# Kernel optimization log

Hardware: AMD Instinct MI355X
Metric: run time of the kernel (lower is better)

## Reference

```python
import jax, jax.numpy as jnp
import numpy as np

BATCH = 16
N_ROIS = 1000
NUM_CLASSES = 81
DET_MAX = 100
MIN_CONF = 0.7
NMS_THRESH = 0.3
BBOX_STD = jnp.array([0.1, 0.1, 0.2, 0.2], jnp.float32)


def setup_inputs() -> dict:
    key = jax.random.key(0)
    k1, k2, k3, k4, k5 = jax.random.split(key, 5)
    # valid normalized boxes (y1,x1,y2,x2) with y2>y1, x2>x1
    y1 = jax.random.uniform(k1, (BATCH, N_ROIS, 1)) * 0.7
    x1 = jax.random.uniform(k2, (BATCH, N_ROIS, 1)) * 0.7
    hw = jax.random.uniform(k3, (BATCH, N_ROIS, 2)) * 0.28 + 0.02
    rois = jnp.concatenate([y1, x1, y1 + hw[..., :1], x1 + hw[..., 1:]], axis=-1)
    fpn_class = jax.nn.softmax(jax.random.normal(k4, (BATCH, N_ROIS, NUM_CLASSES)) * 2.0, axis=-1)
    fpn_bbox = jax.random.normal(k5, (BATCH, N_ROIS, NUM_CLASSES, 4)) * 0.1
    window = jnp.tile(jnp.array([[0.0, 0.0, 1.0, 1.0]], jnp.float32), (BATCH, 1))
    return {"rois": rois, "fpn_class": fpn_class, "fpn_bbox": fpn_bbox, "window": window}


def apply_box_deltas(boxes, deltas):
    # boxes [N,4] (y1,x1,y2,x2), deltas [N,4] (dy,dx,log dh,log dw)
    h = boxes[:, 2] - boxes[:, 0]
    w = boxes[:, 3] - boxes[:, 1]
    cy = boxes[:, 0] + 0.5 * h
    cx = boxes[:, 1] + 0.5 * w
    cy = cy + deltas[:, 0] * h
    cx = cx + deltas[:, 1] * w
    h = h * jnp.exp(deltas[:, 2])
    w = w * jnp.exp(deltas[:, 3])
    y1 = cy - 0.5 * h
    x1 = cx - 0.5 * w
    return jnp.stack([y1, x1, y1 + h, x1 + w], axis=1)


def clip_boxes(boxes, window):
    wy1, wx1, wy2, wx2 = window[0], window[1], window[2], window[3]
    y1 = jnp.clip(boxes[:, 0], wy1, wy2)
    x1 = jnp.clip(boxes[:, 1], wx1, wx2)
    y2 = jnp.clip(boxes[:, 2], wy1, wy2)
    x2 = jnp.clip(boxes[:, 3], wx1, wx2)
    return jnp.stack([y1, x1, y2, x2], axis=1)


def box_iou(a, b):
    # a [N,4], b [M,4] -> [N,M]
    y1 = jnp.maximum(a[:, None, 0], b[None, :, 0])
    x1 = jnp.maximum(a[:, None, 1], b[None, :, 1])
    y2 = jnp.minimum(a[:, None, 2], b[None, :, 2])
    x2 = jnp.minimum(a[:, None, 3], b[None, :, 3])
    inter = jnp.maximum(y2 - y1, 0.0) * jnp.maximum(x2 - x1, 0.0)
    area_a = (a[:, 2] - a[:, 0]) * (a[:, 3] - a[:, 1])
    area_b = (b[:, 2] - b[:, 0]) * (b[:, 3] - b[:, 1])
    union = area_a[:, None] + area_b[None, :] - inter
    return inter / jnp.maximum(union, 1e-10)


def per_class_nms_mask(boxes, class_ids, scores):
    """boxes [N,4], class_ids [N] int, scores [N] (already -1 where pre-filtered).
    Returns bool [N]: survives greedy per-class NMS (max DET_MAX kept per class)."""
    fg = jnp.arange(1, NUM_CLASSES)                       # [C-1] skip background
    sc = jnp.where(class_ids[None, :] == fg[:, None], scores[None, :], -1.0)  # [C-1,N]
    order = jnp.argsort(-sc, axis=1)                      # [C-1,N] score-desc per class
    iou = box_iou(boxes, boxes)                           # [N,N]
    col = jnp.arange(N_ROIS)
    active0 = sc >= 0.0
    kept0 = jnp.zeros_like(active0)
    cnt0 = jnp.zeros((NUM_CLASSES - 1,), jnp.int32)

    def body(i, carry):
        active, kept, cnt = carry
        cur = order[:, i]                                  # [C-1] current box idx per class
        is_act = jnp.take_along_axis(active, cur[:, None], axis=1)[:, 0]
        is_kept = is_act & (cnt < DET_MAX)
        cnt = cnt + is_kept.astype(jnp.int32)
        kept = kept | ((col[None, :] == cur[:, None]) & is_kept[:, None])
        suppress = is_kept[:, None] & (iou[cur] > NMS_THRESH)  # [C-1,N]
        active = active & ~suppress
        return (active, kept, cnt)

    _, kept, _ = jax.lax.fori_loop(0, N_ROIS, body, (active0, kept0, cnt0))
    return kept.any(axis=0)


def _refine_one(rois, probs, deltas, window):
    n = jnp.arange(N_ROIS)
    class_ids = jnp.argmax(probs, axis=1)                 # [N]
    class_scores = probs[n, class_ids]                    # [N]
    d = deltas[n, class_ids] * BBOX_STD                   # [N,4]
    refined = clip_boxes(apply_box_deltas(rois, d), window)
    keep = (class_ids > 0) & (class_scores >= MIN_CONF)
    sg = jax.lax.stop_gradient
    nms_keep = per_class_nms_mask(
        sg(refined), class_ids, jnp.where(keep, sg(class_scores), -1.0))
    keep = keep & nms_keep
    sf = jnp.where(keep, class_scores, -1.0)
    top_s, top_i = jax.lax.top_k(sf, DET_MAX)             # keep top DET_MAX overall
    valid = top_s >= 0.0
    det = jnp.concatenate(
        [refined[top_i],
         class_ids[top_i][:, None].astype(jnp.float32),
         class_scores[top_i][:, None]], axis=1)           # [DET_MAX,6]
    return jnp.where(valid[:, None], det, 0.0)            # zero-pad invalid rows


def reference(rois, fpn_class, fpn_bbox, window):
    # [B, DET_MAX, 6] = (y1,x1,y2,x2,class_id,score), normalized coords
    return jax.vmap(_refine_one)(rois, fpn_class, fpn_bbox, window)
```

## Files before the change

### kernel.cpp

```cpp
#include <hip/hip_runtime.h>
#include <math.h>

#define BATCH 16
#define N_ROIS 1000
#define NUM_CLASSES 81
#define DET_MAX 100
#define MIN_CONF 0.7f
#define NMS_THRESH 0.3f

#define ROI_TILE 128
#define CMAX N_ROIS

__global__ __launch_bounds__(256) void refine_v2(
    const float* __restrict__ rois, const float* __restrict__ probs,
    const float* __restrict__ deltas, const float* __restrict__ window,
    float* __restrict__ ws_box, float* __restrict__ ws_score, int* __restrict__ ws_cls)
{
    __shared__ float s_probs[ROI_TILE * NUM_CLASSES];

    const int tile = blockIdx.x;
    const int base_roi = tile * ROI_TILE;

    const float4* src = (const float4*)(probs + (size_t)base_roi * NUM_CLASSES);
    float4* dst = (float4*)s_probs;
    for (int i = threadIdx.x; i < ROI_TILE * NUM_CLASSES / 4; i += 256)
        dst[i] = src[i];
    __syncthreads();

    if (threadIdx.x < ROI_TILE) {
        const int idx = base_roi + threadIdx.x;
        const int b = idx / N_ROIS;

        const float* p = s_probs + threadIdx.x * NUM_CLASSES;
        int best = 0;
        float bs = p[0];
        for (int c = 1; c < NUM_CLASSES; ++c) {
            float v = p[c];
            if (v > bs) { bs = v; best = c; }
        }

        const float4 dd = ((const float4*)deltas)[(size_t)idx * NUM_CLASSES + best];
        float dy = dd.x * 0.1f, dx = dd.y * 0.1f, dh = dd.z * 0.2f, dw = dd.w * 0.2f;

        const float4 rr = ((const float4*)rois)[idx];
        float y1 = rr.x, x1 = rr.y, y2 = rr.z, x2 = rr.w;
        float h = y2 - y1, w = x2 - x1;
        float cy = y1 + 0.5f * h, cx = x1 + 0.5f * w;
        cy += dy * h;
        cx += dx * w;
        h *= expf(dh);
        w *= expf(dw);
        float ny1 = cy - 0.5f * h;
        float nx1 = cx - 0.5f * w;
        float ny2 = ny1 + h;
        float nx2 = nx1 + w;

        const float* win = window + b * 4;
        float wy1 = win[0], wx1 = win[1], wy2 = win[2], wx2 = win[3];
        ny1 = fminf(fmaxf(ny1, wy1), wy2);
        nx1 = fminf(fmaxf(nx1, wx1), wx2);
        ny2 = fminf(fmaxf(ny2, wy1), wy2);
        nx2 = fminf(fmaxf(nx2, wx1), wx2);

        bool keep = (best > 0) && (bs >= MIN_CONF);

        float4* wbx = (float4*)ws_box;
        wbx[idx] = make_float4(ny1, nx1, ny2, nx2);
        ws_score[idx] = keep ? bs : -1.0f;
        ws_cls[idx] = best;
    }
}

__global__ __launch_bounds__(256) void nms_topk_v2(
    const float* __restrict__ ws_box, const float* __restrict__ ws_score,
    const int* __restrict__ ws_cls, float* __restrict__ out)
{
    const int b = blockIdx.x;
    const int tid = threadIdx.x;

    __shared__ float s_cbox[CMAX][4];
    __shared__ float s_csc[CMAX];
    __shared__ short s_cidx[CMAX];
    __shared__ unsigned char s_ccls[CMAX];
    __shared__ float s_sbox[CMAX][4];
    __shared__ float s_ssc[CMAX];
    __shared__ unsigned char s_scls[CMAX];
    __shared__ unsigned char s_supp[CMAX];
    __shared__ unsigned char s_kept[CMAX];
    __shared__ short s_slot[CMAX];
    __shared__ int s_cnt[NUM_CLASSES];
    __shared__ int s_C;

    if (tid == 0) s_C = 0;
    if (tid < NUM_CLASSES) s_cnt[tid] = 0;

    for (int i = tid; i < DET_MAX * 6; i += 256)
        out[(size_t)b * DET_MAX * 6 + i] = 0.0f;
    __syncthreads();

    for (int i = tid; i < N_ROIS; i += 256) {
        float sc = ws_score[b * N_ROIS + i];
        if (sc >= 0.0f) {
            int k = atomicAdd(&s_C, 1);
            s_csc[k] = sc;
            s_cidx[k] = (short)i;
            s_ccls[k] = (unsigned char)ws_cls[b * N_ROIS + i];
            float4 bb = ((const float4*)ws_box)[b * N_ROIS + i];
            s_cbox[k][0] = bb.x; s_cbox[k][1] = bb.y;
            s_cbox[k][2] = bb.z; s_cbox[k][3] = bb.w;
        }
    }
    __syncthreads();
    const int C = s_C;

    for (int k = tid; k < C; k += 256) {
        float sk = s_csc[k];
        int ik = s_cidx[k];
        int rank = 0;
        for (int j = 0; j < C; ++j) {
            float sj = s_csc[j];
            rank += (sj > sk) | ((sj == sk) & (s_cidx[j] < ik));
        }
        s_ssc[rank] = sk;
        s_scls[rank] = s_ccls[k];
        s_sbox[rank][0] = s_cbox[k][0];
        s_sbox[rank][1] = s_cbox[k][1];
        s_sbox[rank][2] = s_cbox[k][2];
        s_sbox[rank][3] = s_cbox[k][3];
        s_supp[rank] = 0;
        s_kept[rank] = 0;
        s_slot[rank] = 0;
    }
    __syncthreads();

    if (tid < 64) {
        int total = 0;
        for (int i = 0; i < C; ++i) {
            if (s_supp[i]) continue;
            int c = s_scls[i];
            int cn = s_cnt[c];
            if (cn >= DET_MAX) continue;
            s_cnt[c] = cn + 1;
            if (tid == 0) { s_kept[i] = 1; s_slot[i] = (short)total; }
            ++total;
            float a0 = s_sbox[i][0], a1 = s_sbox[i][1];
            float a2 = s_sbox[i][2], a3 = s_sbox[i][3];
            float area_a = (a2 - a0) * (a3 - a1);
            for (int j = i + 1 + tid; j < C; j += 64) {
                if (s_supp[j] || s_scls[j] != c) continue;
                float b0 = s_sbox[j][0], b1 = s_sbox[j][1];
                float b2 = s_sbox[j][2], b3 = s_sbox[j][3];
                float yy1 = fmaxf(a0, b0);
                float xx1 = fmaxf(a1, b1);
                float yy2 = fminf(a2, b2);
                float xx2 = fminf(a3, b3);
                float inter = fmaxf(yy2 - yy1, 0.0f) * fmaxf(xx2 - xx1, 0.0f);
                float area_b = (b2 - b0) * (b3 - b1);
                float uni = area_a + area_b - inter;
                float iou = inter / fmaxf(uni, 1e-10f);
                if (iou > NMS_THRESH) s_supp[j] = 1;
            }
            if (total == DET_MAX) break;
        }
    }
    __syncthreads();

    for (int i = tid; i < C; i += 256) {
        if (s_kept[i]) {
            int slot = s_slot[i];
            float* o = out + (size_t)b * DET_MAX * 6 + slot * 6;
            o[0] = s_sbox[i][0];
            o[1] = s_sbox[i][1];
            o[2] = s_sbox[i][2];
            o[3] = s_sbox[i][3];
            o[4] = (float)s_scls[i];
            o[5] = s_ssc[i];
        }
    }
}

extern "C" void kernel_launch(void* const* d_in, const int* in_sizes, int n_in,
                              void* d_out, int out_size, void* d_ws, size_t ws_size,
                              hipStream_t stream) {
    const float* rois      = (const float*)d_in[0];
    const float* fpn_class = (const float*)d_in[1];
    const float* fpn_bbox  = (const float*)d_in[2];
    const float* window    = (const float*)d_in[3];
    float* out = (float*)d_out;

    float* ws_box   = (float*)d_ws;
    float* ws_score = ws_box + (size_t)BATCH * N_ROIS * 4;
    int*   ws_cls   = (int*)(ws_score + (size_t)BATCH * N_ROIS);

    refine_v2<<<BATCH * N_ROIS / ROI_TILE, 256, 0, stream>>>(
        rois, fpn_class, fpn_bbox, window, ws_box, ws_score, ws_cls);
    nms_topk_v2<<<BATCH, 256, 0, stream>>>(ws_box, ws_score, ws_cls, out);
}
```

Baseline: 94.99 us.

## Fuse refine and NMS into one per-batch kernel with tiled probs staging

Merges the per-roi refinement kernel into the NMS kernel so each batch item is processed by one 1024-thread block that streams class probabilities through shared memory in tiles. Box refinement and delta loads are skipped for rois that fail the confidence filter, and the global workspace round trip and second launch are removed. The cost is much less parallelism for the bandwidth-heavy argmax stage, since only 16 blocks read all probabilities with per-tile barriers.

```diff
diff --git a/kernel.cpp b/kernel.cpp
--- a/kernel.cpp
+++ b/kernel.cpp
@@ -8,112 +8,97 @@
 #define MIN_CONF 0.7f
 #define NMS_THRESH 0.3f
 
-#define ROI_TILE 128
-#define CMAX N_ROIS
+#define TILE_ROIS 200
+#define N_TILES (N_ROIS / TILE_ROIS)
+#define TILE_F4 (TILE_ROIS * NUM_CLASSES / 4)
+#define BLOCK 1024
 
-__global__ __launch_bounds__(256) void refine_v2(
+__global__ __launch_bounds__(BLOCK) void detection_fused(
     const float* __restrict__ rois, const float* __restrict__ probs,
     const float* __restrict__ deltas, const float* __restrict__ window,
-    float* __restrict__ ws_box, float* __restrict__ ws_score, int* __restrict__ ws_cls)
-{
-    __shared__ float s_probs[ROI_TILE * NUM_CLASSES];
-
-    const int tile = blockIdx.x;
-    const int base_roi = tile * ROI_TILE;
-
-    const float4* src = (const float4*)(probs + (size_t)base_roi * NUM_CLASSES);
-    float4* dst = (float4*)s_probs;
-    for (int i = threadIdx.x; i < ROI_TILE * NUM_CLASSES / 4; i += 256)
-        dst[i] = src[i];
-    __syncthreads();
-
-    if (threadIdx.x < ROI_TILE) {
-        const int idx = base_roi + threadIdx.x;
-        const int b = idx / N_ROIS;
-
-        const float* p = s_probs + threadIdx.x * NUM_CLASSES;
-        int best = 0;
-        float bs = p[0];
-        for (int c = 1; c < NUM_CLASSES; ++c) {
-            float v = p[c];
-            if (v > bs) { bs = v; best = c; }
-        }
-
-        const float4 dd = ((const float4*)deltas)[(size_t)idx * NUM_CLASSES + best];
-        float dy = dd.x * 0.1f, dx = dd.y * 0.1f, dh = dd.z * 0.2f, dw = dd.w * 0.2f;
-
-        const float4 rr = ((const float4*)rois)[idx];
-        float y1 = rr.x, x1 = rr.y, y2 = rr.z, x2 = rr.w;
-        float h = y2 - y1, w = x2 - x1;
-        float cy = y1 + 0.5f * h, cx = x1 + 0.5f * w;
-        cy += dy * h;
-        cx += dx * w;
-        h *= expf(dh);
-        w *= expf(dw);
-        float ny1 = cy - 0.5f * h;
-        float nx1 = cx - 0.5f * w;
-        float ny2 = ny1 + h;
-        float nx2 = nx1 + w;
-
-        const float* win = window + b * 4;
-        float wy1 = win[0], wx1 = win[1], wy2 = win[2], wx2 = win[3];
-        ny1 = fminf(fmaxf(ny1, wy1), wy2);
-        nx1 = fminf(fmaxf(nx1, wx1), wx2);
-        ny2 = fminf(fmaxf(ny2, wy1), wy2);
-        nx2 = fminf(fmaxf(nx2, wx1), wx2);
-
-        bool keep = (best > 0) && (bs >= MIN_CONF);
-
-        float4* wbx = (float4*)ws_box;
-        wbx[idx] = make_float4(ny1, nx1, ny2, nx2);
-        ws_score[idx] = keep ? bs : -1.0f;
-        ws_cls[idx] = best;
-    }
-}
-
-__global__ __launch_bounds__(256) void nms_topk_v2(
-    const float* __restrict__ ws_box, const float* __restrict__ ws_score,
-    const int* __restrict__ ws_cls, float* __restrict__ out)
+    float* __restrict__ out)
 {
     const int b = blockIdx.x;
     const int tid = threadIdx.x;
 
-    __shared__ float s_cbox[CMAX][4];
-    __shared__ float s_csc[CMAX];
-    __shared__ short s_cidx[CMAX];
-    __shared__ unsigned char s_ccls[CMAX];
-    __shared__ float s_sbox[CMAX][4];
-    __shared__ float s_ssc[CMAX];
-    __shared__ unsigned char s_scls[CMAX];
-    __shared__ unsigned char s_supp[CMAX];
-    __shared__ unsigned char s_kept[CMAX];
-    __shared__ short s_slot[CMAX];
+    __shared__ float s_tile[TILE_ROIS * NUM_CLASSES];
+    __shared__ float s_cbox[N_ROIS][4];
+    __shared__ float s_csc[N_ROIS];
+    __shared__ short s_cidx[N_ROIS];
+    __shared__ unsigned char s_ccls[N_ROIS];
+    __shared__ float s_sbox[N_ROIS][4];
+    __shared__ float s_ssc[N_ROIS];
+    __shared__ unsigned char s_scls[N_ROIS];
+    __shared__ unsigned char s_supp[N_ROIS];
+    __shared__ unsigned char s_kept[N_ROIS];
+    __shared__ short s_slot[N_ROIS];
     __shared__ int s_cnt[NUM_CLASSES];
     __shared__ int s_C;
 
     if (tid == 0) s_C = 0;
     if (tid < NUM_CLASSES) s_cnt[tid] = 0;
 
-    for (int i = tid; i < DET_MAX * 6; i += 256)
+    for (int i = tid; i < DET_MAX * 6; i += BLOCK)
         out[(size_t)b * DET_MAX * 6 + i] = 0.0f;
-    __syncthreads();
 
-    for (int i = tid; i < N_ROIS; i += 256) {
-        float sc = ws_score[b * N_ROIS + i];
-        if (sc >= 0.0f) {
-            int k = atomicAdd(&s_C, 1);
-            s_csc[k] = sc;
-            s_cidx[k] = (short)i;
-            s_ccls[k] = (unsigned char)ws_cls[b * N_ROIS + i];
-            float4 bb = ((const float4*)ws_box)[b * N_ROIS + i];
-            s_cbox[k][0] = bb.x; s_cbox[k][1] = bb.y;
-            s_cbox[k][2] = bb.z; s_cbox[k][3] = bb.w;
+    const float* win = window + b * 4;
+    const float wy1 = win[0], wx1 = win[1], wy2 = win[2], wx2 = win[3];
+
+    const float4* pbase = (const float4*)(probs + (size_t)b * N_ROIS * NUM_CLASSES);
+
+    for (int t = 0; t < N_TILES; ++t) {
+        const float4* src = pbase + (size_t)t * TILE_F4;
+        float4* dst = (float4*)s_tile;
+        for (int i = tid; i < TILE_F4; i += BLOCK)
+            dst[i] = src[i];
+        __syncthreads();
+
+        if (tid < TILE_ROIS) {
+            const int r = t * TILE_ROIS + tid;
+            const float* p = s_tile + tid * NUM_CLASSES;
+            int best = 0;
+            float bs = p[0];
+            for (int c = 1; c < NUM_CLASSES; ++c) {
+                float v = p[c];
+                if (v > bs) { bs = v; best = c; }
+            }
+
+            if (best > 0 && bs >= MIN_CONF) {
+                const int gidx = b * N_ROIS + r;
+                const float4 dd = ((const float4*)deltas)[(size_t)gidx * NUM_CLASSES + best];
+                float dy = dd.x * 0.1f, dx = dd.y * 0.1f, dh = dd.z * 0.2f, dw = dd.w * 0.2f;
+
+                const float4 rr = ((const float4*)rois)[gidx];
+                float y1 = rr.x, x1 = rr.y, y2 = rr.z, x2 = rr.w;
+                float h = y2 - y1, w = x2 - x1;
+                float cy = y1 + 0.5f * h, cx = x1 + 0.5f * w;
+                cy += dy * h;
+                cx += dx * w;
+                h *= expf(dh);
+                w *= expf(dw);
+                float ny1 = cy - 0.5f * h;
+                float nx1 = cx - 0.5f * w;
+                float ny2 = ny1 + h;
+                float nx2 = nx1 + w;
+
+                ny1 = fminf(fmaxf(ny1, wy1), wy2);
+                nx1 = fminf(fmaxf(nx1, wx1), wx2);
+                ny2 = fminf(fmaxf(ny2, wy1), wy2);
+                nx2 = fminf(fmaxf(nx2, wx1), wx2);
+
+                int k = atomicAdd(&s_C, 1);
+                s_cbox[k][0] = ny1; s_cbox[k][1] = nx1;
+                s_cbox[k][2] = ny2; s_cbox[k][3] = nx2;
+                s_csc[k] = bs;
+                s_cidx[k] = (short)r;
+                s_ccls[k] = (unsigned char)best;
+            }
         }
+        __syncthreads();
     }
-    __syncthreads();
     const int C = s_C;
 
-    for (int k = tid; k < C; k += 256) {
+    for (int k = tid; k < C; k += BLOCK) {
         float sk = s_csc[k];
         int ik = s_cidx[k];
         int rank = 0;
@@ -157,18 +142,16 @@
                 float inter = fmaxf(yy2 - yy1, 0.0f) * fmaxf(xx2 - xx1, 0.0f);
                 float area_b = (b2 - b0) * (b3 - b1);
                 float uni = area_a + area_b - inter;
-                float iou = inter / fmaxf(uni, 1e-10f);
-                if (iou > NMS_THRESH) s_supp[j] = 1;
+                if (inter / fmaxf(uni, 1e-10f) > NMS_THRESH) s_supp[j] = 1;
             }
             if (total == DET_MAX) break;
         }
     }
     __syncthreads();
 
-    for (int i = tid; i < C; i += 256) {
+    for (int i = tid; i < C; i += BLOCK) {
         if (s_kept[i]) {
-            int slot = s_slot[i];
-            float* o = out + (size_t)b * DET_MAX * 6 + slot * 6;
+            float* o = out + (size_t)b * DET_MAX * 6 + s_slot[i] * 6;
             o[0] = s_sbox[i][0];
             o[1] = s_sbox[i][1];
             o[2] = s_sbox[i][2];
@@ -188,11 +171,6 @@
     const float* window    = (const float*)d_in[3];
     float* out = (float*)d_out;
 
-    float* ws_box   = (float*)d_ws;
-    float* ws_score = ws_box + (size_t)BATCH * N_ROIS * 4;
-    int*   ws_cls   = (int*)(ws_score + (size_t)BATCH * N_ROIS);
-
-    refine_v2<<<BATCH * N_ROIS / ROI_TILE, 256, 0, stream>>>(
-        rois, fpn_class, fpn_bbox, window, ws_box, ws_score, ws_cls);
-    nms_topk_v2<<<BATCH, 256, 0, stream>>>(ws_box, ws_score, ws_cls, out);
+    detection_fused<<<BATCH, BLOCK, 0, stream>>>(
+        rois, fpn_class, fpn_bbox, window, out);
 }
```

After: 102.6 us. 1.08x slower.

## Parallelize NMS across classes with per-class buckets and skip refine for dropped ROIs

Applied to the files above, without the earlier changes.

The serial greedy NMS loop, run by one wavefront over all candidates, is replaced by per-class buckets: a prefix sum gives class offsets, and each class runs its own NMS on one thread against earlier kept boxes in the same class. Output slots come from counting kept entries before each index. The refine kernel now computes and stores boxes and class only for ROIs that pass the confidence filter, which avoids the gather from the deltas tensor for dropped ROIs. Within a class the work is serial per thread and the bucket fill scans all candidates, so load imbalance between classes is possible.

```diff
diff --git a/kernel.cpp b/kernel.cpp
--- a/kernel.cpp
+++ b/kernel.cpp
@@ -9,17 +9,15 @@
 #define NMS_THRESH 0.3f
 
 #define ROI_TILE 128
-#define CMAX N_ROIS
-
-__global__ __launch_bounds__(256) void refine_v2(
+
+__global__ __launch_bounds__(256) void refine_v3(
     const float* __restrict__ rois, const float* __restrict__ probs,
     const float* __restrict__ deltas, const float* __restrict__ window,
     float* __restrict__ ws_box, float* __restrict__ ws_score, int* __restrict__ ws_cls)
 {
     __shared__ float s_probs[ROI_TILE * NUM_CLASSES];
 
-    const int tile = blockIdx.x;
-    const int base_roi = tile * ROI_TILE;
+    const int base_roi = blockIdx.x * ROI_TILE;
 
     const float4* src = (const float4*)(probs + (size_t)base_roi * NUM_CLASSES);
     float4* dst = (float4*)s_probs;
@@ -39,56 +37,57 @@
             if (v > bs) { bs = v; best = c; }
         }
 
-        const float4 dd = ((const float4*)deltas)[(size_t)idx * NUM_CLASSES + best];
-        float dy = dd.x * 0.1f, dx = dd.y * 0.1f, dh = dd.z * 0.2f, dw = dd.w * 0.2f;
-
-        const float4 rr = ((const float4*)rois)[idx];
-        float y1 = rr.x, x1 = rr.y, y2 = rr.z, x2 = rr.w;
-        float h = y2 - y1, w = x2 - x1;
-        float cy = y1 + 0.5f * h, cx = x1 + 0.5f * w;
-        cy += dy * h;
-        cx += dx * w;
-        h *= expf(dh);
-        w *= expf(dw);
-        float ny1 = cy - 0.5f * h;
-        float nx1 = cx - 0.5f * w;
-        float ny2 = ny1 + h;
-        float nx2 = nx1 + w;
-
-        const float* win = window + b * 4;
-        float wy1 = win[0], wx1 = win[1], wy2 = win[2], wx2 = win[3];
-        ny1 = fminf(fmaxf(ny1, wy1), wy2);
-        nx1 = fminf(fmaxf(nx1, wx1), wx2);
-        ny2 = fminf(fmaxf(ny2, wy1), wy2);
-        nx2 = fminf(fmaxf(nx2, wx1), wx2);
-
-        bool keep = (best > 0) && (bs >= MIN_CONF);
-
-        float4* wbx = (float4*)ws_box;
-        wbx[idx] = make_float4(ny1, nx1, ny2, nx2);
+        const bool keep = (best > 0) && (bs >= MIN_CONF);
         ws_score[idx] = keep ? bs : -1.0f;
-        ws_cls[idx] = best;
+
+        if (keep) {
+            const float4 dd = ((const float4*)deltas)[(size_t)idx * NUM_CLASSES + best];
+            float dy = dd.x * 0.1f, dx = dd.y * 0.1f, dh = dd.z * 0.2f, dw = dd.w * 0.2f;
+
+            const float4 rr = ((const float4*)rois)[idx];
+            float y1 = rr.x, x1 = rr.y, y2 = rr.z, x2 = rr.w;
+            float h = y2 - y1, w = x2 - x1;
+            float cy = y1 + 0.5f * h, cx = x1 + 0.5f * w;
+            cy += dy * h;
+            cx += dx * w;
+            h *= expf(dh);
+            w *= expf(dw);
+            float ny1 = cy - 0.5f * h;
+            float nx1 = cx - 0.5f * w;
+            float ny2 = ny1 + h;
+            float nx2 = nx1 + w;
+
+            const float* win = window + b * 4;
+            float wy1 = win[0], wx1 = win[1], wy2 = win[2], wx2 = win[3];
+            ny1 = fminf(fmaxf(ny1, wy1), wy2);
+            nx1 = fminf(fmaxf(nx1, wx1), wx2);
+            ny2 = fminf(fmaxf(ny2, wy1), wy2);
+            nx2 = fminf(fmaxf(nx2, wx1), wx2);
+
+            ((float4*)ws_box)[idx] = make_float4(ny1, nx1, ny2, nx2);
+            ws_cls[idx] = best;
+        }
     }
 }
 
-__global__ __launch_bounds__(256) void nms_topk_v2(
+__global__ __launch_bounds__(256) void nms_v3(
     const float* __restrict__ ws_box, const float* __restrict__ ws_score,
     const int* __restrict__ ws_cls, float* __restrict__ out)
 {
     const int b = blockIdx.x;
     const int tid = threadIdx.x;
 
-    __shared__ float s_cbox[CMAX][4];
-    __shared__ float s_csc[CMAX];
-    __shared__ short s_cidx[CMAX];
-    __shared__ unsigned char s_ccls[CMAX];
-    __shared__ float s_sbox[CMAX][4];
-    __shared__ float s_ssc[CMAX];
-    __shared__ unsigned char s_scls[CMAX];
-    __shared__ unsigned char s_supp[CMAX];
-    __shared__ unsigned char s_kept[CMAX];
-    __shared__ short s_slot[CMAX];
+    __shared__ float s_cbox[N_ROIS][4];
+    __shared__ float s_csc[N_ROIS];
+    __shared__ short s_cidx[N_ROIS];
+    __shared__ unsigned char s_ccls[N_ROIS];
+    __shared__ float s_sbox[N_ROIS][4];
+    __shared__ float s_ssc[N_ROIS];
+    __shared__ unsigned char s_scls[N_ROIS];
+    __shared__ unsigned char s_kept[N_ROIS];
+    __shared__ short s_bucket[N_ROIS];
     __shared__ int s_cnt[NUM_CLASSES];
+    __shared__ int s_off[NUM_CLASSES];
     __shared__ int s_C;
 
     if (tid == 0) s_C = 0;
@@ -104,7 +103,9 @@
             int k = atomicAdd(&s_C, 1);
             s_csc[k] = sc;
             s_cidx[k] = (short)i;
-            s_ccls[k] = (unsigned char)ws_cls[b * N_ROIS + i];
+            int c = ws_cls[b * N_ROIS + i];
+            s_ccls[k] = (unsigned char)c;
+            atomicAdd(&s_cnt[c], 1);
             float4 bb = ((const float4*)ws_box)[b * N_ROIS + i];
             s_cbox[k][0] = bb.x; s_cbox[k][1] = bb.y;
             s_cbox[k][2] = bb.z; s_cbox[k][3] = bb.w;
@@ -127,54 +128,64 @@
         s_sbox[rank][1] = s_cbox[k][1];
         s_sbox[rank][2] = s_cbox[k][2];
         s_sbox[rank][3] = s_cbox[k][3];
-        s_supp[rank] = 0;
         s_kept[rank] = 0;
-        s_slot[rank] = 0;
-    }
-    __syncthreads();
-
-    if (tid < 64) {
-        int total = 0;
-        for (int i = 0; i < C; ++i) {
-            if (s_supp[i]) continue;
-            int c = s_scls[i];
-            int cn = s_cnt[c];
-            if (cn >= DET_MAX) continue;
-            s_cnt[c] = cn + 1;
-            if (tid == 0) { s_kept[i] = 1; s_slot[i] = (short)total; }
-            ++total;
-            float a0 = s_sbox[i][0], a1 = s_sbox[i][1];
-            float a2 = s_sbox[i][2], a3 = s_sbox[i][3];
-            float area_a = (a2 - a0) * (a3 - a1);
-            for (int j = i + 1 + tid; j < C; j += 64) {
-                if (s_supp[j] || s_scls[j] != c) continue;
-                float b0 = s_sbox[j][0], b1 = s_sbox[j][1];
-                float b2 = s_sbox[j][2], b3 = s_sbox[j][3];
+    }
+    if (tid == 0) {
+        int acc = 0;
+        for (int c = 0; c < NUM_CLASSES; ++c) { s_off[c] = acc; acc += s_cnt[c]; }
+    }
+    __syncthreads();
+
+    if (tid >= 1 && tid < NUM_CLASSES) {
+        int p = s_off[tid];
+        for (int i = 0; i < C; ++i)
+            if (s_scls[i] == tid) s_bucket[p++] = (short)i;
+    }
+    __syncthreads();
+
+    if (tid >= 1 && tid < NUM_CLASSES) {
+        const int off = s_off[tid];
+        const int m = s_cnt[tid];
+        int kept_cnt = 0;
+        for (int a = 0; a < m; ++a) {
+            if (kept_cnt >= DET_MAX) break;
+            int i = s_bucket[off + a];
+            float b0 = s_sbox[i][0], b1 = s_sbox[i][1];
+            float b2 = s_sbox[i][2], b3 = s_sbox[i][3];
+            float area_b = (b2 - b0) * (b3 - b1);
+            bool sup = false;
+            for (int q = 0; q < a; ++q) {
+                int j = s_bucket[off + q];
+                if (!s_kept[j]) continue;
+                float a0 = s_sbox[j][0], a1 = s_sbox[j][1];
+                float a2 = s_sbox[j][2], a3 = s_sbox[j][3];
                 float yy1 = fmaxf(a0, b0);
                 float xx1 = fmaxf(a1, b1);
                 float yy2 = fminf(a2, b2);
                 float xx2 = fminf(a3, b3);
                 float inter = fmaxf(yy2 - yy1, 0.0f) * fmaxf(xx2 - xx1, 0.0f);
-                float area_b = (b2 - b0) * (b3 - b1);
+                float area_a = (a2 - a0) * (a3 - a1);
                 float uni = area_a + area_b - inter;
-                float iou = inter / fmaxf(uni, 1e-10f);
-                if (iou > NMS_THRESH) s_supp[j] = 1;
+                if (inter / fmaxf(uni, 1e-10f) > NMS_THRESH) { sup = true; break; }
             }
-            if (total == DET_MAX) break;
+            if (!sup) { s_kept[i] = 1; ++kept_cnt; }
         }
     }
     __syncthreads();
 
     for (int i = tid; i < C; i += 256) {
         if (s_kept[i]) {
-            int slot = s_slot[i];
-            float* o = out + (size_t)b * DET_MAX * 6 + slot * 6;
-            o[0] = s_sbox[i][0];
-            o[1] = s_sbox[i][1];
-            o[2] = s_sbox[i][2];
-            o[3] = s_sbox[i][3];
-            o[4] = (float)s_scls[i];
-            o[5] = s_ssc[i];
+            int slot = 0;
+            for (int j = 0; j < i; ++j) slot += s_kept[j];
+            if (slot < DET_MAX) {
+                float* o = out + (size_t)b * DET_MAX * 6 + slot * 6;
+                o[0] = s_sbox[i][0];
+                o[1] = s_sbox[i][1];
+                o[2] = s_sbox[i][2];
+                o[3] = s_sbox[i][3];
+                o[4] = (float)s_scls[i];
+                o[5] = s_ssc[i];
+            }
         }
     }
 }
@@ -192,7 +203,7 @@
     float* ws_score = ws_box + (size_t)BATCH * N_ROIS * 4;
     int*   ws_cls   = (int*)(ws_score + (size_t)BATCH * N_ROIS);
 
-    refine_v2<<<BATCH * N_ROIS / ROI_TILE, 256, 0, stream>>>(
+    refine_v3<<<BATCH * N_ROIS / ROI_TILE, 256, 0, stream>>>(
         rois, fpn_class, fpn_bbox, window, ws_box, ws_score, ws_cls);
-    nms_topk_v2<<<BATCH, 256, 0, stream>>>(ws_box, ws_score, ws_cls, out);
+    nms_v3<<<BATCH, 256, 0, stream>>>(ws_box, ws_score, ws_cls, out);
 }
```

Result: faster. 88.45 us (-6.9%).
